# Performance work log

Measured on AMD Instinct MI355X. Metric: run time of the kernel, lower is better.

## Reference

```python
import jax, jax.numpy as jnp
import numpy as np

NUM_LAYERS = 5
EMB_DIM = 300
NUM_ATOM_TYPE = 121
NUM_CHIRALITY = 11
NUM_BOND_TYPE = 7
NUM_BOND_DIR = 3
BN_EPS = 1e-5


def setup_inputs() -> dict:
    key = jax.random.key(0)
    ks = jax.random.split(key, 16)
    N, E, D, L = 100000, 200000, EMB_DIM, NUM_LAYERS

    def glorot(k, shape):
        fan_in, fan_out = shape[-2], shape[-1]
        s = jnp.sqrt(6.0 / (fan_in + fan_out))
        return jax.random.uniform(k, shape, jnp.float32, -s, s)

    x = jax.random.randint(ks[0], (N, 2), 0, 11)  # atom type / chirality (both < 11, in range)
    edge_index = jax.random.randint(ks[1], (2, E), 0, N)
    edge_attr = jax.random.randint(ks[2], (E, 2), 0, 3)

    return {
        "x": x,
        "edge_index": edge_index,
        "edge_attr": edge_attr,
        "x_emb1": glorot(ks[3], (NUM_ATOM_TYPE, D)),
        "x_emb2": glorot(ks[4], (NUM_CHIRALITY, D)),
        "edge_emb1": glorot(ks[5], (L, NUM_BOND_TYPE, D)),
        "edge_emb2": glorot(ks[6], (L, NUM_BOND_DIR, D)),
        "w1": glorot(ks[7], (L, D, 2 * D)),
        "b1": jnp.zeros((L, 2 * D), jnp.float32),
        "w2": glorot(ks[8], (L, 2 * D, D)),
        "b2": jnp.zeros((L, D), jnp.float32),
        "bn_gamma": jnp.ones((L, D), jnp.float32),
        "bn_beta": jnp.zeros((L, D), jnp.float32),
    }


def reference(x, edge_index, edge_attr, x_emb1, x_emb2, edge_emb1, edge_emb2,
              w1, b1, w2, b2, bn_gamma, bn_beta):
    N = x.shape[0]
    # GINConv.forward adds self loops with edge_attr row [4, 0]
    loop = jnp.arange(N)
    src = jnp.concatenate([edge_index[0], loop])  # [E+N]
    dst = jnp.concatenate([edge_index[1], loop])  # [E+N]
    ea0 = jnp.concatenate([edge_attr[:, 0], jnp.full((N,), 4, edge_attr.dtype)])
    ea1 = jnp.concatenate([edge_attr[:, 1], jnp.zeros((N,), edge_attr.dtype)])

    # node input embedding
    h = x_emb1[x[:, 0]] + x_emb2[x[:, 1]]  # [N, D]

    for l in range(NUM_LAYERS):
        # edge embeddings (incl. self loops)
        eemb = edge_emb1[l][ea0] + edge_emb2[l][ea1]  # [E+N, D]
        # message: x_j + edge_attr, aggr='add' at destination nodes
        msg = h[src] + eemb
        agg = jax.ops.segment_sum(msg, dst, num_segments=N)  # [N, D]
        # GIN update MLP: Linear(D, 2D) -> ReLU -> Linear(2D, D)
        h2 = jax.nn.relu(agg @ w1[l] + b1[l]) @ w2[l] + b2[l]
        # BatchNorm1d (training mode: batch statistics, biased variance)
        mean = h2.mean(axis=0)
        var = h2.var(axis=0)
        h2 = (h2 - mean) * jax.lax.rsqrt(var + BN_EPS) * bn_gamma[l] + bn_beta[l]
        # ReLU on all but last layer (dropout is identity, drop_ratio=0)
        if l < NUM_LAYERS - 1:
            h2 = jax.nn.relu(h2)
        h = h2
    # JK == 'last'
    return h
```

## Files before the change

### kernel.cpp

```cpp
#include <hip/hip_runtime.h>
#include <hip/hip_bf16.h>
#include <stdint.h>

typedef __bf16 bf16_t;
typedef bf16_t bf16x8 __attribute__((ext_vector_type(8)));
typedef float  f32x4  __attribute__((ext_vector_type(4)));

__global__ void embed_kernel(const int* __restrict__ x, const float* __restrict__ e1,
                             const float* __restrict__ e2, bf16_t* __restrict__ h, int N) {
  const int w = (blockIdx.x * blockDim.x + threadIdx.x) >> 6;
  const int lane = threadIdx.x & 63;
  if (w >= N || lane >= 40) return;
  const int t0 = x[2 * w], t1 = x[2 * w + 1];
  const int co = lane * 8;
  f32x4 a0 = *(const f32x4*)&e1[t0 * 300 + co];
  f32x4 a1 = *(const f32x4*)&e1[t0 * 300 + co + 4];
  f32x4 b0 = *(const f32x4*)&e2[t1 * 300 + co];
  f32x4 b1 = *(const f32x4*)&e2[t1 * 300 + co + 4];
  bf16x8 o;
  #pragma unroll
  for (int j = 0; j < 8; j++) {
    float v = (j < 4) ? (a0[j] + b0[j]) : (a1[j - 4] + b1[j - 4]);
    o[j] = (co + j < 300) ? (bf16_t)v : (bf16_t)0.f;
  }
  *(bf16x8*)&h[(size_t)w * 320 + co] = o;
}

__global__ void count_deg_kernel(const int* __restrict__ ei, int* __restrict__ deg, int E) {
  int e = blockIdx.x * 256 + threadIdx.x;
  if (e < E) atomicAdd(&deg[ei[E + e]], 1);
}

__global__ void scan_partial_kernel(const int* __restrict__ deg, int* __restrict__ part, int N) {
  __shared__ int s[256];
  const int tid = threadIdx.x;
  const int idx = blockIdx.x * 256 + tid;
  s[tid] = (idx < N) ? deg[idx] : 0;
  __syncthreads();
  for (int off = 128; off > 0; off >>= 1) {
    if (tid < off) s[tid] += s[tid + off];
    __syncthreads();
  }
  if (tid == 0) part[blockIdx.x] = s[0];
}

__global__ void scan_block_kernel(int* __restrict__ part, int n) {
  __shared__ int s[1024];
  const int tid = threadIdx.x;
  const int v = (tid < n) ? part[tid] : 0;
  s[tid] = v;
  __syncthreads();
  for (int off = 1; off < 1024; off <<= 1) {
    int x = (tid >= off) ? s[tid - off] : 0;
    __syncthreads();
    s[tid] += x;
    __syncthreads();
  }
  if (tid < n) part[tid] = s[tid] - v;
}

__global__ void scan_final_kernel(const int* __restrict__ deg, const int* __restrict__ part,
                                  int* __restrict__ rowptr, int* __restrict__ cursor, int N, int E) {
  __shared__ int s[256];
  const int tid = threadIdx.x;
  const int idx = blockIdx.x * 256 + tid;
  const int v = (idx < N) ? deg[idx] : 0;
  s[tid] = v;
  __syncthreads();
  for (int off = 1; off < 256; off <<= 1) {
    int x = (tid >= off) ? s[tid - off] : 0;
    __syncthreads();
    s[tid] += x;
    __syncthreads();
  }
  if (idx < N) {
    int ex = s[tid] - v + part[blockIdx.x];
    rowptr[idx] = ex;
    cursor[idx] = ex;
  }
  if (idx == 0) rowptr[N] = E;
}

__global__ void fill_csr_kernel(const int* __restrict__ ei, const int* __restrict__ ea,
                                int* __restrict__ cursor, int* __restrict__ epack, int E) {
  int e = blockIdx.x * 256 + threadIdx.x;
  if (e >= E) return;
  int slot = atomicAdd(&cursor[ei[E + e]], 1);
  int a = ea[2 * e] * 3 + ea[2 * e + 1];
  epack[slot] = (ei[e] & 0xFFFFF) | (a << 20);
}

__global__ void convert_w1_kernel(const float* __restrict__ w1, bf16_t* __restrict__ o) {
  int id = blockIdx.x * 256 + threadIdx.x;
  if (id >= 5 * 640 * 320) return;
  int k = id % 320;
  int n = (id / 320) % 640;
  int l = id / (320 * 640);
  float v = (k < 300 && n < 600) ? w1[(size_t)l * 300 * 600 + (size_t)k * 600 + n] : 0.f;
  o[id] = (bf16_t)v;
}

__global__ void convert_w2_kernel(const float* __restrict__ w2, bf16_t* __restrict__ o) {
  int id = blockIdx.x * 256 + threadIdx.x;
  if (id >= 5 * 384 * 640) return;
  int k = id % 640;
  int n = (id / 640) % 384;
  int l = id / (640 * 384);
  float v = (k < 600 && n < 300) ? w2[(size_t)l * 600 * 300 + (size_t)k * 300 + n] : 0.f;
  o[id] = (bf16_t)v;
}

__global__ void build_t12_kernel(const float* __restrict__ ee1, const float* __restrict__ ee2,
                                 bf16_t* __restrict__ T12) {
  int id = blockIdx.x * 256 + threadIdx.x;
  if (id >= 5 * 21 * 320) return;
  int col = id % 320;
  int r = id / 320;
  int l = r / 21;
  int a = r % 21;
  int a0 = a / 3, a1 = a % 3;
  float v = 0.f;
  if (col < 300) v = ee1[((size_t)l * 7 + a0) * 300 + col] + ee2[((size_t)l * 3 + a1) * 300 + col];
  T12[id] = (bf16_t)v;
}

template <bool FUSE_BN>
__global__ void aggregate_kernel(const bf16_t* __restrict__ hsrc, const int* __restrict__ rowptr,
                                 const int* __restrict__ epack, const bf16_t* __restrict__ T12L,
                                 const float* __restrict__ scale, const float* __restrict__ shift,
                                 bf16_t* __restrict__ agg, int N, int LDH) {
  const int g = blockIdx.x * 256 + threadIdx.x;
  const int w = g / 40;
  if (w >= N) return;
  const int co = (g - w * 40) * 8;

  float sc[8], sh[8];
  if (FUSE_BN) {
    f32x4 s0 = *(const f32x4*)&scale[co];
    f32x4 s1 = *(const f32x4*)&scale[co + 4];
    f32x4 t0 = *(const f32x4*)&shift[co];
    f32x4 t1 = *(const f32x4*)&shift[co + 4];
    #pragma unroll
    for (int j = 0; j < 4; j++) { sc[j] = s0[j]; sc[j + 4] = s1[j]; sh[j] = t0[j]; sh[j + 4] = t1[j]; }
  }

  const int beg = rowptr[w], end = rowptr[w + 1];
  float acc[8];
  {
    bf16x8 hv = *(const bf16x8*)&hsrc[(size_t)w * LDH + co];
    bf16x8 tv = *(const bf16x8*)&T12L[12 * 320 + co];
    #pragma unroll
    for (int j = 0; j < 8; j++) {
      float v = (float)hv[j];
      if (FUSE_BN) v = fmaxf(v * sc[j] + sh[j], 0.f);
      acc[j] = v + (float)tv[j];
    }
  }
  for (int e = beg; e < end; e++) {
    const int p = epack[e];
    const int s = p & 0xFFFFF;
    const int a = (p >> 20) & 0x1F;
    bf16x8 hv = *(const bf16x8*)&hsrc[(size_t)s * LDH + co];
    bf16x8 tv = *(const bf16x8*)&T12L[a * 320 + co];
    #pragma unroll
    for (int j = 0; j < 8; j++) {
      float v = (float)hv[j];
      if (FUSE_BN) v = fmaxf(v * sc[j] + sh[j], 0.f);
      acc[j] += v + (float)tv[j];
    }
  }
  bf16x8 o;
  #pragma unroll
  for (int j = 0; j < 8; j++) o[j] = (bf16_t)acc[j];
  *(bf16x8*)&agg[(size_t)w * 320 + co] = o;
}

template <int LDA, int LDB, int LDC, int NK, int GY, int NBIAS, bool RELU, bool STATS>
__global__ __launch_bounds__(256, 3) void gemm_kernel(const bf16_t* __restrict__ A,
                                                      const bf16_t* __restrict__ BT,
                                                      const float* __restrict__ bias,
                                                      bf16_t* __restrict__ C,
                                                      float* __restrict__ sums,
                                                      float* __restrict__ sumsq,
                                                      int Nvalid, int nwg) {
  __shared__ __align__(16) bf16_t As0[128 * 32];
  __shared__ __align__(16) bf16_t Bs0[128 * 32];
  __shared__ __align__(16) bf16_t As1[128 * 32];
  __shared__ __align__(16) bf16_t Bs1[128 * 32];

  const int tid = threadIdx.x;
  const int lane = tid & 63;
  const int wave = tid >> 6;
  const int ml = lane & 15, quad = lane >> 4;
  const int wm = (wave & 1) * 64, wn = (wave >> 1) * 64;
  const int kx = (ml >> 1) & 3;

  const int bid = blockIdx.x;
  const int q = nwg >> 3, r = nwg & 7;
  const int xcd = bid & 7, pos = bid >> 3;
  const int logical = (xcd < r ? xcd * (q + 1) : r * (q + 1) + (xcd - r) * q) + pos;
  const size_t bm = (size_t)(logical / GY) * 128;
  const size_t bnn = (size_t)(logical % GY) * 128;

  const int srow = tid >> 2;
  const int cg = (tid & 3) ^ ((tid >> 3) & 3);
  const bf16_t* ag = A + (bm + srow) * LDA + cg * 8;
  const bf16_t* bg = BT + (bnn + srow) * LDB + cg * 8;

  auto loadA = [&](int kb, bf16x8& r0, bf16x8& r1) {
    const int kof = kb * 32;
    r0 = *(const bf16x8*)(ag + kof);
    r1 = *(const bf16x8*)(ag + (size_t)64 * LDA + kof);
  };
  auto loadB = [&](int kb, bf16x8& r0, bf16x8& r1) {
    const int kof = kb * 32;
    r0 = *(const bf16x8*)(bg + kof);
    r1 = *(const bf16x8*)(bg + (size_t)64 * LDB + kof);
  };
  auto store = [&](bf16_t* as, bf16_t* bs, const bf16x8& a0, const bf16x8& a1,
                   const bf16x8& b0, const bf16x8& b1) {
    *(bf16x8*)&as[(size_t)tid * 8] = a0;
    *(bf16x8*)&as[(256 + (size_t)tid) * 8] = a1;
    *(bf16x8*)&bs[(size_t)tid * 8] = b0;
    *(bf16x8*)&bs[(256 + (size_t)tid) * 8] = b1;
  };

  f32x4 acc[4][4];
  #pragma unroll
  for (int rr = 0; rr < 4; rr++)
    #pragma unroll
    for (int cc = 0; cc < 4; cc++) acc[rr][cc] = (f32x4){0.f, 0.f, 0.f, 0.f};

  auto compute = [&](const bf16_t* as, const bf16_t* bs) {
    const int ck = quad ^ kx;
    bf16x8 aF[4], bF[4];
    #pragma unroll
    for (int mf = 0; mf < 4; mf++)
      aF[mf] = *(const bf16x8*)&as[((wm + mf * 16 + ml) * 4 + ck) * 8];
    #pragma unroll
    for (int nf = 0; nf < 4; nf++)
      bF[nf] = *(const bf16x8*)&bs[((wn + nf * 16 + ml) * 4 + ck) * 8];
    #pragma unroll
    for (int mf = 0; mf < 4; mf++)
      #pragma unroll
      for (int nf = 0; nf < 4; nf++)
        acc[mf][nf] = __builtin_amdgcn_mfma_f32_16x16x32_bf16(aF[mf], bF[nf], acc[mf][nf], 0, 0, 0);
  };

  bf16x8 a[2][2], b[2];
  loadA(0, a[0][0], a[0][1]);
  loadB(0, b[0], b[1]);
  loadA(1, a[1][0], a[1][1]);
  store(As0, Bs0, a[0][0], a[0][1], b[0], b[1]);
  asm volatile("s_waitcnt lgkmcnt(0)" ::: "memory");
  __builtin_amdgcn_s_barrier();
  __builtin_amdgcn_sched_barrier(0);

  #pragma unroll
  for (int kb = 0; kb < NK; kb++) {
    if (kb + 1 < NK) loadB(kb + 1, b[0], b[1]);
    if (kb + 2 < NK) loadA(kb + 2, a[kb % 2][0], a[kb % 2][1]);
    if ((kb & 1) == 0) compute(As0, Bs0); else compute(As1, Bs1);
    if (kb + 1 < NK) {
      if ((kb & 1) == 0) store(As1, Bs1, a[(kb + 1) % 2][0], a[(kb + 1) % 2][1], b[0], b[1]);
      else               store(As0, Bs0, a[(kb + 1) % 2][0], a[(kb + 1) % 2][1], b[0], b[1]);
      asm volatile("s_waitcnt lgkmcnt(0)" ::: "memory");
      __builtin_amdgcn_s_barrier();
      __builtin_amdgcn_sched_barrier(0);
    }
  }

  #pragma unroll
  for (int nf = 0; nf < 4; nf++) {
    const int colg = (int)bnn + wn + nf * 16 + ml;
    const float bv = (colg < NBIAS) ? bias[colg] : 0.f;
    float s = 0.f, sq = 0.f;
    #pragma unroll
    for (int mf = 0; mf < 4; mf++) {
      #pragma unroll
      for (int i = 0; i < 4; i++) {
        const size_t rowg = bm + wm + mf * 16 + quad * 4 + i;
        float v = acc[mf][nf][i] + bv;
        if (RELU) v = fmaxf(v, 0.f);
        C[rowg * LDC + colg] = (bf16_t)v;
        if (STATS) {
          const bool ok = rowg < (size_t)Nvalid;
          s += ok ? v : 0.f;
          sq += ok ? v * v : 0.f;
        }
      }
    }
    if (STATS) {
      s += __shfl_down(s, 16);
      sq += __shfl_down(sq, 16);
      s += __shfl_down(s, 32);
      sq += __shfl_down(sq, 32);
      if (quad == 0) {
        atomicAdd(&sums[colg], s);
        atomicAdd(&sumsq[colg], sq);
      }
    }
  }
}

__global__ void bn_params_kernel(const float* __restrict__ sums, const float* __restrict__ sumsq,
                                 const float* __restrict__ gamma, const float* __restrict__ beta,
                                 float* __restrict__ scale, float* __restrict__ shift, int N) {
  const int col = threadIdx.x;
  if (col >= 384) return;
  if (col >= 300) {
    scale[col] = 0.f;
    shift[col] = 0.f;
    return;
  }
  const float inv = 1.f / (float)N;
  const float mean = sums[col] * inv;
  float var = sumsq[col] * inv - mean * mean;
  if (var < 0.f) var = 0.f;
  const float sc = gamma[col] * rsqrtf(var + 1e-5f);
  scale[col] = sc;
  shift[col] = beta[col] - mean * sc;
}

__global__ void bn_apply_kernel(const bf16_t* __restrict__ H2, const float* __restrict__ scale,
                                const float* __restrict__ shift, float* __restrict__ out, int N) {
  const int w = (blockIdx.x * blockDim.x + threadIdx.x) >> 6;
  const int lane = threadIdx.x & 63;
  if (w >= N || lane >= 40) return;
  const int co = lane * 8;
  bf16x8 v8 = *(const bf16x8*)&H2[(size_t)w * 384 + co];
  f32x4 s0 = *(const f32x4*)&scale[co];
  f32x4 s1 = *(const f32x4*)&scale[co + 4];
  f32x4 t0 = *(const f32x4*)&shift[co];
  f32x4 t1 = *(const f32x4*)&shift[co + 4];
  #pragma unroll
  for (int j = 0; j < 8; j++) {
    float sc = (j < 4) ? s0[j] : s1[j - 4];
    float sh = (j < 4) ? t0[j] : t1[j - 4];
    float v = (float)v8[j] * sc + sh;
    if (co + j < 300) out[(size_t)w * 300 + co + j] = v;
  }
}

extern "C" void kernel_launch(void* const* d_in, const int* in_sizes, int n_in,
                              void* d_out, int out_size, void* d_ws, size_t ws_size,
                              hipStream_t stream) {
  const int* x = (const int*)d_in[0];
  const int* ei = (const int*)d_in[1];
  const int* ea = (const int*)d_in[2];
  const float* xe1 = (const float*)d_in[3];
  const float* xe2 = (const float*)d_in[4];
  const float* ee1 = (const float*)d_in[5];
  const float* ee2 = (const float*)d_in[6];
  const float* w1 = (const float*)d_in[7];
  const float* b1 = (const float*)d_in[8];
  const float* w2 = (const float*)d_in[9];
  const float* b2 = (const float*)d_in[10];
  const float* gam = (const float*)d_in[11];
  const float* bet = (const float*)d_in[12];

  const int N = in_sizes[0] / 2;
  const int E = in_sizes[1] / 2;
  const int Mt = (N + 127) / 128;
  const size_t Mp = (size_t)Mt * 128;

  char* p = (char*)d_ws;
  auto take = [&](size_t b) -> char* {
    char* r = p;
    p += (b + 255) & ~(size_t)255;
    return r;
  };
  bf16_t* h    = (bf16_t*)take(Mp * 320 * 2);
  bf16_t* agg  = (bf16_t*)take(Mp * 320 * 2);
  bf16_t* C1   = (bf16_t*)take(Mp * 640 * 2);
  bf16_t* H2   = (bf16_t*)take(Mp * 384 * 2);
  bf16_t* W1bT = (bf16_t*)take((size_t)5 * 640 * 320 * 2);
  bf16_t* W2bT = (bf16_t*)take((size_t)5 * 384 * 640 * 2);
  bf16_t* T12  = (bf16_t*)take((size_t)5 * 21 * 320 * 2);
  int* deg     = (int*)take((size_t)N * 4);
  int* rowptr  = (int*)take((size_t)(N + 1) * 4);
  int* cursor  = (int*)take((size_t)N * 4);
  int* part    = (int*)take(1024 * 4);
  int* epack   = (int*)take((size_t)E * 4);
  float* sums  = (float*)take(384 * 4);
  float* sumsq = (float*)take(384 * 4);
  float* scale = (float*)take(384 * 4);
  float* shift = (float*)take(384 * 4);

  hipMemsetAsync(agg, 0, Mp * 320 * 2, stream);
  hipMemsetAsync(deg, 0, (size_t)N * 4, stream);

  const int nwb = (N + 3) / 4;
  embed_kernel<<<nwb, 256, 0, stream>>>(x, xe1, xe2, h, N);

  count_deg_kernel<<<(E + 255) / 256, 256, 0, stream>>>(ei, deg, E);
  const int nsb = (N + 255) / 256;
  scan_partial_kernel<<<nsb, 256, 0, stream>>>(deg, part, N);
  scan_block_kernel<<<1, 1024, 0, stream>>>(part, nsb);
  scan_final_kernel<<<nsb, 256, 0, stream>>>(deg, part, rowptr, cursor, N, E);
  fill_csr_kernel<<<(E + 255) / 256, 256, 0, stream>>>(ei, ea, cursor, epack, E);

  convert_w1_kernel<<<(5 * 640 * 320 + 255) / 256, 256, 0, stream>>>(w1, W1bT);
  convert_w2_kernel<<<(5 * 384 * 640 + 255) / 256, 256, 0, stream>>>(w2, W2bT);
  build_t12_kernel<<<(5 * 21 * 320 + 255) / 256, 256, 0, stream>>>(ee1, ee2, T12);

  const int nwg1 = Mt * 5;
  const int nwg2 = Mt * 3;
  const int nab = (N * 40 + 255) / 256;

  for (int l = 0; l < 5; l++) {
    if (l == 0) {
      aggregate_kernel<false><<<nab, 256, 0, stream>>>(h, rowptr, epack,
                                                       T12 + (size_t)l * 21 * 320,
                                                       scale, shift, agg, N, 320);
    } else {
      aggregate_kernel<true><<<nab, 256, 0, stream>>>(H2, rowptr, epack,
                                                      T12 + (size_t)l * 21 * 320,
                                                      scale, shift, agg, N, 384);
    }
    gemm_kernel<320, 320, 640, 10, 5, 600, true, false>
        <<<nwg1, 256, 0, stream>>>(agg, W1bT + (size_t)l * 640 * 320,
                                   b1 + (size_t)l * 600, C1, sums, sumsq, N, nwg1);
    hipMemsetAsync(sums, 0, 384 * 4, stream);
    hipMemsetAsync(sumsq, 0, 384 * 4, stream);
    gemm_kernel<640, 640, 384, 20, 3, 300, false, true>
        <<<nwg2, 256, 0, stream>>>(C1, W2bT + (size_t)l * 384 * 640,
                                   b2 + (size_t)l * 300, H2, sums, sumsq, N, nwg2);
    bn_params_kernel<<<1, 384, 0, stream>>>(sums, sumsq, gam + (size_t)l * 300,
                                            bet + (size_t)l * 300, scale, shift, N);
  }
  bn_apply_kernel<<<nwb, 256, 0, stream>>>(H2, scale, shift, (float*)d_out, N);
}
```

Baseline: 1.367 ms.

## Load GEMM MFMA fragments directly from global memory, dropping LDS staging

The GEMM kernel no longer stages A and B tiles through double-buffered shared memory with barriers. Each wave now loads its MFMA operand fragments straight from global memory into registers, double-buffered across k-steps. This removes LDS writes and reads and the workgroup barriers, but each tile is fetched several times by different waves (relying on L1/L2 for reuse), and the loads are less coalesced.

```diff
diff --git a/kernel.cpp b/kernel.cpp
--- a/kernel.cpp
+++ b/kernel.cpp
@@ -183,17 +183,11 @@
                                                       float* __restrict__ sums,
                                                       float* __restrict__ sumsq,
                                                       int Nvalid, int nwg) {
-  __shared__ __align__(16) bf16_t As0[128 * 32];
-  __shared__ __align__(16) bf16_t Bs0[128 * 32];
-  __shared__ __align__(16) bf16_t As1[128 * 32];
-  __shared__ __align__(16) bf16_t Bs1[128 * 32];
-
   const int tid = threadIdx.x;
   const int lane = tid & 63;
   const int wave = tid >> 6;
   const int ml = lane & 15, quad = lane >> 4;
   const int wm = (wave & 1) * 64, wn = (wave >> 1) * 64;
-  const int kx = (ml >> 1) & 3;
 
   const int bid = blockIdx.x;
   const int q = nwg >> 3, r = nwg & 7;
@@ -202,28 +196,8 @@
   const size_t bm = (size_t)(logical / GY) * 128;
   const size_t bnn = (size_t)(logical % GY) * 128;
 
-  const int srow = tid >> 2;
-  const int cg = (tid & 3) ^ ((tid >> 3) & 3);
-  const bf16_t* ag = A + (bm + srow) * LDA + cg * 8;
-  const bf16_t* bg = BT + (bnn + srow) * LDB + cg * 8;
-
-  auto loadA = [&](int kb, bf16x8& r0, bf16x8& r1) {
-    const int kof = kb * 32;
-    r0 = *(const bf16x8*)(ag + kof);
-    r1 = *(const bf16x8*)(ag + (size_t)64 * LDA + kof);
-  };
-  auto loadB = [&](int kb, bf16x8& r0, bf16x8& r1) {
-    const int kof = kb * 32;
-    r0 = *(const bf16x8*)(bg + kof);
-    r1 = *(const bf16x8*)(bg + (size_t)64 * LDB + kof);
-  };
-  auto store = [&](bf16_t* as, bf16_t* bs, const bf16x8& a0, const bf16x8& a1,
-                   const bf16x8& b0, const bf16x8& b1) {
-    *(bf16x8*)&as[(size_t)tid * 8] = a0;
-    *(bf16x8*)&as[(256 + (size_t)tid) * 8] = a1;
-    *(bf16x8*)&bs[(size_t)tid * 8] = b0;
-    *(bf16x8*)&bs[(256 + (size_t)tid) * 8] = b1;
-  };
+  const bf16_t* aB = A + (bm + wm + ml) * LDA + quad * 8;
+  const bf16_t* bB = BT + (bnn + wn + ml) * LDB + quad * 8;
 
   f32x4 acc[4][4];
   #pragma unroll
@@ -231,43 +205,29 @@
     #pragma unroll
     for (int cc = 0; cc < 4; cc++) acc[rr][cc] = (f32x4){0.f, 0.f, 0.f, 0.f};
 
-  auto compute = [&](const bf16_t* as, const bf16_t* bs) {
-    const int ck = quad ^ kx;
-    bf16x8 aF[4], bF[4];
-    #pragma unroll
-    for (int mf = 0; mf < 4; mf++)
-      aF[mf] = *(const bf16x8*)&as[((wm + mf * 16 + ml) * 4 + ck) * 8];
-    #pragma unroll
-    for (int nf = 0; nf < 4; nf++)
-      bF[nf] = *(const bf16x8*)&bs[((wn + nf * 16 + ml) * 4 + ck) * 8];
+  bf16x8 aR[2][4], bR[2][4];
+  #pragma unroll
+  for (int mf = 0; mf < 4; mf++) aR[0][mf] = *(const bf16x8*)(aB + (size_t)mf * 16 * LDA);
+  #pragma unroll
+  for (int nf = 0; nf < 4; nf++) bR[0][nf] = *(const bf16x8*)(bB + (size_t)nf * 16 * LDB);
+
+  #pragma unroll
+  for (int kb = 0; kb < NK; kb++) {
+    const int cur = kb & 1, nxt = cur ^ 1;
+    if (kb + 1 < NK) {
+      #pragma unroll
+      for (int mf = 0; mf < 4; mf++)
+        aR[nxt][mf] = *(const bf16x8*)(aB + (size_t)mf * 16 * LDA + (kb + 1) * 32);
+      #pragma unroll
+      for (int nf = 0; nf < 4; nf++)
+        bR[nxt][nf] = *(const bf16x8*)(bB + (size_t)nf * 16 * LDB + (kb + 1) * 32);
+    }
     #pragma unroll
     for (int mf = 0; mf < 4; mf++)
       #pragma unroll
       for (int nf = 0; nf < 4; nf++)
-        acc[mf][nf] = __builtin_amdgcn_mfma_f32_16x16x32_bf16(aF[mf], bF[nf], acc[mf][nf], 0, 0, 0);
-  };
-
-  bf16x8 a[2][2], b[2];
-  loadA(0, a[0][0], a[0][1]);
-  loadB(0, b[0], b[1]);
-  loadA(1, a[1][0], a[1][1]);
-  store(As0, Bs0, a[0][0], a[0][1], b[0], b[1]);
-  asm volatile("s_waitcnt lgkmcnt(0)" ::: "memory");
-  __builtin_amdgcn_s_barrier();
-  __builtin_amdgcn_sched_barrier(0);
-
-  #pragma unroll
-  for (int kb = 0; kb < NK; kb++) {
-    if (kb + 1 < NK) loadB(kb + 1, b[0], b[1]);
-    if (kb + 2 < NK) loadA(kb + 2, a[kb % 2][0], a[kb % 2][1]);
-    if ((kb & 1) == 0) compute(As0, Bs0); else compute(As1, Bs1);
-    if (kb + 1 < NK) {
-      if ((kb & 1) == 0) store(As1, Bs1, a[(kb + 1) % 2][0], a[(kb + 1) % 2][1], b[0], b[1]);
-      else               store(As0, Bs0, a[(kb + 1) % 2][0], a[(kb + 1) % 2][1], b[0], b[1]);
-      asm volatile("s_waitcnt lgkmcnt(0)" ::: "memory");
-      __builtin_amdgcn_s_barrier();
-      __builtin_amdgcn_sched_barrier(0);
-    }
+        acc[mf][nf] = __builtin_amdgcn_mfma_f32_16x16x32_bf16(aR[cur][mf], bR[cur][nf],
+                                                              acc[mf][nf], 0, 0, 0);
   }
 
   #pragma unroll
```

Result: slower. 2.395 ms (+75.2%).
